# Optimization experiments

Hardware: AMD Instinct MI355X
Metric: run time of the kernel (lower is better)

Reference implementation:

```python
import jax, jax.numpy as jnp
import numpy as np


def setup_inputs() -> dict:
    key = jax.random.key(0)
    k1, k2, k3 = jax.random.split(key, 3)
    B, H, W = 4, 1024, 1024
    D, Hg, Wg = 8, 16, 16
    C = 12  # (Cin+1)*Cout = (3+1)*3
    grid = jax.random.normal(k1, (B, C, D, Hg, Wg), dtype=jnp.float32)
    guide = jax.random.uniform(k2, (B, H, W), dtype=jnp.float32)
    image = jax.random.normal(k3, (B, 3, H, W), dtype=jnp.float32)
    return {"grid": grid, "guide": guide, "image": image}


def _slice_coeffs(grid, guide):
    """Guide-indexed trilinear slice of the bilateral grid.

    grid:  [B, C, D, Hg, Wg]; guide: [B, H, W] in [0,1].
    Returns per-pixel coefficients [B, H, W, C].
    """
    B, C, D, Hg, Wg = grid.shape
    _, H, W = guide.shape
    grid_t = jnp.transpose(grid, (0, 2, 3, 4, 1))  # [B, D, Hg, Wg, C]

    # grid-space coordinates of each pixel (HDRNet convention)
    gx = (jnp.arange(W, dtype=grid.dtype) + 0.5) * Wg / W   # [W]
    gy = (jnp.arange(H, dtype=grid.dtype) + 0.5) * Hg / H   # [H]
    gz = guide * D                                          # [B, H, W]

    fx = jnp.floor(gx - 0.5)
    fy = jnp.floor(gy - 0.5)
    fz = jnp.floor(gz - 0.5)

    bb = jnp.arange(B)[:, None, None]
    coeff = jnp.zeros((B, H, W, C), dtype=grid.dtype)
    for dz in (0, 1):
        zz = fz + dz
        wz = jnp.maximum(1.0 - jnp.abs(zz + 0.5 - gz), 0.0)     # [B,H,W]
        zi = jnp.clip(zz, 0, D - 1).astype(jnp.int32)
        for dy in (0, 1):
            yy = fy + dy
            wy = jnp.maximum(1.0 - jnp.abs(yy + 0.5 - gy), 0.0)  # [H]
            yi = jnp.clip(yy, 0, Hg - 1).astype(jnp.int32)
            for dx in (0, 1):
                xx = fx + dx
                wx = jnp.maximum(1.0 - jnp.abs(xx + 0.5 - gx), 0.0)  # [W]
                xi = jnp.clip(xx, 0, Wg - 1).astype(jnp.int32)
                w = wz * wy[None, :, None] * wx[None, None, :]       # [B,H,W]
                c = grid_t[bb, zi, yi[None, :, None], xi[None, None, :]]  # [B,H,W,C]
                coeff = coeff + w[..., None] * c
    return coeff


def reference(grid, guide, image):
    B, Cin, H, W = image.shape
    coeff = _slice_coeffs(grid, guide)                 # [B,H,W,(Cin+1)*Cout]
    Cout = coeff.shape[-1] // (Cin + 1)
    coeff = coeff.reshape(B, H, W, Cout, Cin + 1)
    # per-pixel affine: out[c] = sum_j A[c,j] * image[j] + bias[c]
    out = jnp.einsum('bhwcj,bjhw->bchw', coeff[..., :Cin], image)
    out = out + jnp.transpose(coeff[..., Cin], (0, 3, 1, 2))
    return out
```

## Files before the change

kernel.cpp:

```cpp
#include <hip/hip_runtime.h>

#define BB 4
#define CC 12
#define DD 8
#define HG 16
#define WG 16
#define HH 1024
#define WW 1024

typedef float vf4 __attribute__((ext_vector_type(4)));

#define XSTRIDE 104
#define ROWS 2

__global__ __launch_bounds__(256) void slice_apply(
    const float* __restrict__ grid,
    const float* __restrict__ guide,
    const float* __restrict__ img,
    float* __restrict__ out)
{
    __shared__ float S[ROWS * WG * XSTRIDE];

    const int blk = blockIdx.x;
    const int b  = blk >> 9;
    const int h0 = (blk & 511) * ROWS;

    const float gy0 = (h0 + 0.5f) * ((float)HG / (float)HH);
    const float fy  = floorf(gy0 - 0.5f);
    const int   iy0 = max(0, min(HG - 1, (int)fy));
    const int   iy1 = max(0, min(HG - 1, (int)fy + 1));

    float wy1r[ROWS];
    #pragma unroll
    for (int r = 0; r < ROWS; ++r) {
        const float gy = (h0 + r + 0.5f) * ((float)HG / (float)HH);
        wy1r[r] = gy - 0.5f - fy;
    }

    for (int j = threadIdx.x; j < CC * DD * WG; j += 256) {
        const int x = j & 15;
        const int z = (j >> 4) & 7;
        const int c = j >> 7;
        const size_t base = ((size_t)(b * CC + c) * DD + z) * (HG * WG);
        const float v0 = grid[base + iy0 * WG + x];
        const float v1 = grid[base + iy1 * WG + x];
        const int so = x * XSTRIDE + z * CC + c;
        #pragma unroll
        for (int r = 0; r < ROWS; ++r) {
            const float ty = wy1r[r];
            S[r * (WG * XSTRIDE) + so] = v0 + ty * (v1 - v0);
        }
    }
    __syncthreads();

    const int w0 = threadIdx.x * 4;

    const float scale = (float)WG / (float)WW;
    const float gx0 = (w0 + 0.5f) * scale;
    const float fx  = floorf(gx0 - 0.5f);
    const float tx0 = gx0 - 0.5f - fx;
    const int   ix0 = max(0, min(WG - 1, (int)fx));
    const int   ix1 = max(0, min(WG - 1, (int)fx + 1));

    #pragma unroll
    for (int r = 0; r < ROWS; ++r) {
        const int h = h0 + r;
        const float* Sr  = S + r * (WG * XSTRIDE);
        const float* Sx0 = Sr + ix0 * XSTRIDE;
        const float* Sx1 = Sr + ix1 * XSTRIDE;

        const size_t pix = ((size_t)b * HH + h) * WW + w0;
        const vf4 g4 = *reinterpret_cast<const vf4*>(guide + pix);
        const float* ib = img + (((size_t)b * 3) * HH + h) * WW + w0;
        const vf4 i0 = __builtin_nontemporal_load(reinterpret_cast<const vf4*>(ib));
        const vf4 i1 = __builtin_nontemporal_load(reinterpret_cast<const vf4*>(ib + (size_t)HH * WW));
        const vf4 i2 = __builtin_nontemporal_load(reinterpret_cast<const vf4*>(ib + (size_t)2 * HH * WW));

        vf4 o0, o1, o2;

        #pragma unroll
        for (int p = 0; p < 4; ++p) {
            const float tx  = tx0 + (float)p * scale;
            const float wx0 = 1.0f - tx, wx1 = tx;

            const float gv = g4[p];
            const float gz  = gv * (float)DD;
            const float fz  = floorf(gz - 0.5f);
            const float tz  = gz - 0.5f - fz;
            const int   iz0 = max(0, min(DD - 1, (int)fz));
            const int   iz1 = max(0, min(DD - 1, (int)fz + 1));
            const float wz0 = 1.0f - tz, wz1 = tz;

            const float w00 = wz0 * wx0, w01 = wz0 * wx1;
            const float w10 = wz1 * wx0, w11 = wz1 * wx1;

            float acc[12];
            #pragma unroll
            for (int k = 0; k < 12; ++k) acc[k] = 0.0f;

            auto accum = [&](const float* P, float w) {
                const vf4 a = *reinterpret_cast<const vf4*>(P);
                const vf4 e = *reinterpret_cast<const vf4*>(P + 4);
                const vf4 f = *reinterpret_cast<const vf4*>(P + 8);
                #pragma unroll
                for (int k = 0; k < 4; ++k) {
                    acc[k]     += w * a[k];
                    acc[4 + k] += w * e[k];
                    acc[8 + k] += w * f[k];
                }
            };
            accum(Sx0 + iz0 * CC, w00);
            accum(Sx1 + iz0 * CC, w01);
            accum(Sx0 + iz1 * CC, w10);
            accum(Sx1 + iz1 * CC, w11);

            const float im0 = i0[p];
            const float im1 = i1[p];
            const float im2 = i2[p];

            o0[p] = acc[0] * im0 + acc[1] * im1 + acc[2]  * im2 + acc[3];
            o1[p] = acc[4] * im0 + acc[5] * im1 + acc[6]  * im2 + acc[7];
            o2[p] = acc[8] * im0 + acc[9] * im1 + acc[10] * im2 + acc[11];
        }

        float* ob = out + (((size_t)b * 3) * HH + h) * WW + w0;
        __builtin_nontemporal_store(o0, reinterpret_cast<vf4*>(ob));
        __builtin_nontemporal_store(o1, reinterpret_cast<vf4*>(ob + (size_t)HH * WW));
        __builtin_nontemporal_store(o2, reinterpret_cast<vf4*>(ob + (size_t)2 * HH * WW));
    }
}

extern "C" void kernel_launch(void* const* d_in, const int* in_sizes, int n_in,
                              void* d_out, int out_size, void* d_ws, size_t ws_size,
                              hipStream_t stream) {
    const float* grid  = (const float*)d_in[0];
    const float* guide = (const float*)d_in[1];
    const float* image = (const float*)d_in[2];
    float* out = (float*)d_out;

    const int nblocks = BB * HH / ROWS;
    slice_apply<<<nblocks, 256, 0, stream>>>(grid, guide, image, out);
}
```

Before: 124.1 us.

## Stage y-pair grid slices in fp16 and double-buffer row loads over 8 rows

Each block now covers 8 rows instead of 2. The shared tile holds both y-neighbour grid values as fp16 pairs, and the y interpolation happens per pixel at compute time rather than per row during staging. Guide and image loads for the next row are issued before the current row is computed, so global latency is hidden by software double-buffering. Output stores become plain instead of nontemporal. The cost is fp16 rounding of the grid coefficients, extra FMAs per pixel for the y blend, and fewer blocks overall.

Result: slower. 127.8 us (+2.9%).

```diff
diff --git a/kernel.cpp b/kernel.cpp
--- a/kernel.cpp
+++ b/kernel.cpp
@@ -9,9 +9,11 @@
 #define WW 1024
 
 typedef float vf4 __attribute__((ext_vector_type(4)));
+typedef _Float16 h8 __attribute__((ext_vector_type(8)));
 
-#define XSTRIDE 104
-#define ROWS 2
+#define XSTRH 208
+#define RPB 8
+#define NSTG 12
 
 __global__ __launch_bounds__(256) void slice_apply(
     const float* __restrict__ grid,
@@ -19,41 +21,50 @@
     const float* __restrict__ img,
     float* __restrict__ out)
 {
-    __shared__ float S[ROWS * WG * XSTRIDE];
+    __shared__ _Float16 S[WG * XSTRH];
 
     const int blk = blockIdx.x;
-    const int b  = blk >> 9;
-    const int h0 = (blk & 511) * ROWS;
+    const int b  = blk >> 7;
+    const int h0 = (blk & 127) * RPB;
 
     const float gy0 = (h0 + 0.5f) * ((float)HG / (float)HH);
     const float fy  = floorf(gy0 - 0.5f);
     const int   iy0 = max(0, min(HG - 1, (int)fy));
     const int   iy1 = max(0, min(HG - 1, (int)fy + 1));
 
-    float wy1r[ROWS];
+    float sv[NSTG];
+    int   sw[NSTG];
     #pragma unroll
-    for (int r = 0; r < ROWS; ++r) {
-        const float gy = (h0 + r + 0.5f) * ((float)HG / (float)HH);
-        wy1r[r] = gy - 0.5f - fy;
+    for (int t = 0; t < NSTG; ++t) {
+        const int j = (int)threadIdx.x + t * 256;
+        const int x    = j & 15;
+        const int rest = j >> 4;
+        const int y    = rest & 1;
+        const int zc   = rest >> 1;
+        const int z    = zc & 7;
+        const int c    = zc >> 3;
+        const int iy   = y ? iy1 : iy0;
+        sv[t] = grid[((size_t)(b * CC + c) * DD + z) * (HG * WG) + iy * WG + x];
+        sw[t] = x * XSTRH + z * 24 + c * 2 + y;
     }
 
-    for (int j = threadIdx.x; j < CC * DD * WG; j += 256) {
-        const int x = j & 15;
-        const int z = (j >> 4) & 7;
-        const int c = j >> 7;
-        const size_t base = ((size_t)(b * CC + c) * DD + z) * (HG * WG);
-        const float v0 = grid[base + iy0 * WG + x];
-        const float v1 = grid[base + iy1 * WG + x];
-        const int so = x * XSTRIDE + z * CC + c;
-        #pragma unroll
-        for (int r = 0; r < ROWS; ++r) {
-            const float ty = wy1r[r];
-            S[r * (WG * XSTRIDE) + so] = v0 + ty * (v1 - v0);
-        }
-    }
+    const int w0 = (int)threadIdx.x * 4;
+
+    auto loadrow = [&](int r, vf4& G, vf4& I0, vf4& I1, vf4& I2) {
+        const size_t pix = ((size_t)b * HH + (h0 + r)) * WW + w0;
+        G = *reinterpret_cast<const vf4*>(guide + pix);
+        const float* ib = img + (((size_t)b * 3) * HH + (h0 + r)) * WW + w0;
+        I0 = __builtin_nontemporal_load(reinterpret_cast<const vf4*>(ib));
+        I1 = __builtin_nontemporal_load(reinterpret_cast<const vf4*>(ib + (size_t)HH * WW));
+        I2 = __builtin_nontemporal_load(reinterpret_cast<const vf4*>(ib + (size_t)2 * HH * WW));
+    };
+
+    vf4 gA, a0A, a1A, a2A, gB, a0B, a1B, a2B;
+    loadrow(0, gA, a0A, a1A, a2A);
+
+    #pragma unroll
+    for (int t = 0; t < NSTG; ++t) S[sw[t]] = (_Float16)sv[t];
     __syncthreads();
-
-    const int w0 = threadIdx.x * 4;
 
     const float scale = (float)WG / (float)WW;
     const float gx0 = (w0 + 0.5f) * scale;
@@ -61,72 +72,68 @@
     const float tx0 = gx0 - 0.5f - fx;
     const int   ix0 = max(0, min(WG - 1, (int)fx));
     const int   ix1 = max(0, min(WG - 1, (int)fx + 1));
+    const _Float16* Sx0 = S + ix0 * XSTRH;
+    const _Float16* Sx1 = S + ix1 * XSTRH;
 
-    #pragma unroll
-    for (int r = 0; r < ROWS; ++r) {
+    auto compute = [&](int r, const vf4& G, const vf4& I0, const vf4& I1, const vf4& I2) {
         const int h = h0 + r;
-        const float* Sr  = S + r * (WG * XSTRIDE);
-        const float* Sx0 = Sr + ix0 * XSTRIDE;
-        const float* Sx1 = Sr + ix1 * XSTRIDE;
-
-        const size_t pix = ((size_t)b * HH + h) * WW + w0;
-        const vf4 g4 = *reinterpret_cast<const vf4*>(guide + pix);
-        const float* ib = img + (((size_t)b * 3) * HH + h) * WW + w0;
-        const vf4 i0 = __builtin_nontemporal_load(reinterpret_cast<const vf4*>(ib));
-        const vf4 i1 = __builtin_nontemporal_load(reinterpret_cast<const vf4*>(ib + (size_t)HH * WW));
-        const vf4 i2 = __builtin_nontemporal_load(reinterpret_cast<const vf4*>(ib + (size_t)2 * HH * WW));
+        const float gy = (h + 0.5f) * ((float)HG / (float)HH);
+        const float ty = gy - 0.5f - fy;
+        const float wy0 = 1.0f - ty, wy1 = ty;
 
         vf4 o0, o1, o2;
-
         #pragma unroll
         for (int p = 0; p < 4; ++p) {
             const float tx  = tx0 + (float)p * scale;
             const float wx0 = 1.0f - tx, wx1 = tx;
 
-            const float gv = g4[p];
-            const float gz  = gv * (float)DD;
+            const float gz  = G[p] * (float)DD;
             const float fz  = floorf(gz - 0.5f);
             const float tz  = gz - 0.5f - fz;
-            const int   iz0 = max(0, min(DD - 1, (int)fz));
-            const int   iz1 = max(0, min(DD - 1, (int)fz + 1));
+            const int   ifz = (int)fz;
+            const int   iz0 = max(0, min(DD - 1, ifz));
+            const int   iz1 = max(0, min(DD - 1, ifz + 1));
             const float wz0 = 1.0f - tz, wz1 = tz;
-
-            const float w00 = wz0 * wx0, w01 = wz0 * wx1;
-            const float w10 = wz1 * wx0, w11 = wz1 * wx1;
 
             float acc[12];
             #pragma unroll
             for (int k = 0; k < 12; ++k) acc[k] = 0.0f;
 
-            auto accum = [&](const float* P, float w) {
-                const vf4 a = *reinterpret_cast<const vf4*>(P);
-                const vf4 e = *reinterpret_cast<const vf4*>(P + 4);
-                const vf4 f = *reinterpret_cast<const vf4*>(P + 8);
+            auto accum = [&](const _Float16* P, float w) {
+                const float wa = w * wy0, wb = w * wy1;
+                const h8 v0 = *reinterpret_cast<const h8*>(P);
+                const h8 v1 = *reinterpret_cast<const h8*>(P + 8);
+                const h8 v2 = *reinterpret_cast<const h8*>(P + 16);
                 #pragma unroll
                 for (int k = 0; k < 4; ++k) {
-                    acc[k]     += w * a[k];
-                    acc[4 + k] += w * e[k];
-                    acc[8 + k] += w * f[k];
+                    acc[k]     += wa * (float)v0[2*k] + wb * (float)v0[2*k+1];
+                    acc[4 + k] += wa * (float)v1[2*k] + wb * (float)v1[2*k+1];
+                    acc[8 + k] += wa * (float)v2[2*k] + wb * (float)v2[2*k+1];
                 }
             };
-            accum(Sx0 + iz0 * CC, w00);
-            accum(Sx1 + iz0 * CC, w01);
-            accum(Sx0 + iz1 * CC, w10);
-            accum(Sx1 + iz1 * CC, w11);
+            accum(Sx0 + iz0 * 24, wz0 * wx0);
+            accum(Sx1 + iz0 * 24, wz0 * wx1);
+            accum(Sx0 + iz1 * 24, wz1 * wx0);
+            accum(Sx1 + iz1 * 24, wz1 * wx1);
 
-            const float im0 = i0[p];
-            const float im1 = i1[p];
-            const float im2 = i2[p];
-
+            const float im0 = I0[p], im1 = I1[p], im2 = I2[p];
             o0[p] = acc[0] * im0 + acc[1] * im1 + acc[2]  * im2 + acc[3];
             o1[p] = acc[4] * im0 + acc[5] * im1 + acc[6]  * im2 + acc[7];
             o2[p] = acc[8] * im0 + acc[9] * im1 + acc[10] * im2 + acc[11];
         }
 
         float* ob = out + (((size_t)b * 3) * HH + h) * WW + w0;
-        __builtin_nontemporal_store(o0, reinterpret_cast<vf4*>(ob));
-        __builtin_nontemporal_store(o1, reinterpret_cast<vf4*>(ob + (size_t)HH * WW));
-        __builtin_nontemporal_store(o2, reinterpret_cast<vf4*>(ob + (size_t)2 * HH * WW));
+        *reinterpret_cast<vf4*>(ob) = o0;
+        *reinterpret_cast<vf4*>(ob + (size_t)HH * WW) = o1;
+        *reinterpret_cast<vf4*>(ob + (size_t)2 * HH * WW) = o2;
+    };
+
+    #pragma unroll
+    for (int r = 0; r < RPB; r += 2) {
+        if (r + 1 < RPB) loadrow(r + 1, gB, a0B, a1B, a2B);
+        compute(r, gA, a0A, a1A, a2A);
+        if (r + 2 < RPB) loadrow(r + 2, gA, a0A, a1A, a2A);
+        compute(r + 1, gB, a0B, a1B, a2B);
     }
 }
 
@@ -138,6 +145,6 @@
     const float* image = (const float*)d_in[2];
     float* out = (float*)d_out;
 
-    const int nblocks = BB * HH / ROWS;
+    const int nblocks = BB * HH / RPB;
     slice_apply<<<nblocks, 256, 0, stream>>>(grid, guide, image, out);
 }
```
